# Kernel tuning notes

Hardware: AMD Instinct MI355X
Metric: run time of the kernel (lower is better)

Reference implementation:

```python
import math
import jax, jax.numpy as jnp
import numpy as np

ALPHA, BETA, GAMMA = 1.9, 3.8, 15.2
HEIGHT, WIDTH, SKIP = 32, 32, 1
NUM_HEADS, DIM = 12, 768
HEAD_DIM = DIM // NUM_HEADS


def _piecewise_index_np(rp, alpha, beta, gamma):
    # Eq. (18): identity inside |rp|<=alpha, logarithmic bucketing outside, clipped at beta.
    rp = rp.astype(np.float64)
    rp_abs = np.abs(rp)
    inside = np.round(rp)
    log_part = alpha + np.log(np.maximum(rp_abs, 1e-9) / alpha) / math.log(gamma / alpha) * (beta - alpha)
    outside = np.sign(rp) * np.minimum(np.round(log_part), beta)
    return np.where(rp_abs <= alpha, inside, outside).astype(np.int64)


def _bucket_ids_cross(height, width, skip, alpha, beta, gamma, axis):
    # axis=0 -> CROSS_ROWS, axis=1 -> CROSS_COLS
    rows = np.arange(height)[:, None].repeat(width, 1)
    cols = np.arange(width)[None, :].repeat(height, 0)
    pos = np.stack([rows, cols], 2).reshape(-1, 2)  # [L, 2]
    diff = pos[:, None, axis] - pos[None, :, axis]  # [L, L]
    beta_int = int(beta)
    ids = _piecewise_index_np(diff, alpha, beta, gamma) + beta_int  # in [0, 2*beta_int]
    num_buckets = 2 * beta_int + 1
    L = height * width
    if skip > 0:
        extra = num_buckets
        new_ids = np.full((skip + L, skip + L), extra, dtype=np.int64)
        new_ids[skip:, skip:] = ids
        ids = new_ids
        num_buckets += 1
    return ids.astype(np.int32), num_buckets


def setup_inputs() -> dict:
    key = jax.random.key(0)
    ks = jax.random.split(key, 8)
    N = SKIP + HEIGHT * WIDTH  # 1025
    B = 8
    br, nb = _bucket_ids_cross(HEIGHT, WIDTH, SKIP, ALPHA, BETA, GAMMA, axis=0)
    bc, _ = _bucket_ids_cross(HEIGHT, WIDTH, SKIP, ALPHA, BETA, GAMMA, axis=1)
    w = 0.02
    return {
        "x": jax.random.normal(ks[0], (B, N, DIM), jnp.float32),
        "qkv_w": jax.random.normal(ks[1], (3 * DIM, DIM), jnp.float32) * w,
        "qkv_b": jnp.zeros((3 * DIM,), jnp.float32),
        "proj_w": jax.random.normal(ks[2], (DIM, DIM), jnp.float32) * w,
        "proj_b": jnp.zeros((DIM,), jnp.float32),
        "rpe_rows": jax.random.normal(ks[3], (NUM_HEADS, nb, HEAD_DIM), jnp.float32) * w,
        "rpe_cols": jax.random.normal(ks[4], (NUM_HEADS, nb, HEAD_DIM), jnp.float32) * w,
        "bucket_rows": jnp.asarray(br),
        "bucket_cols": jnp.asarray(bc),
    }


def reference(x, qkv_w, qkv_b, proj_w, proj_b, rpe_rows, rpe_cols, bucket_rows, bucket_cols):
    B, N, C = x.shape
    h = rpe_rows.shape[0]
    d = C // h
    scale = d ** -0.5
    qkv = (x @ qkv_w.T + qkv_b).reshape(B, N, 3, h, d).transpose(2, 0, 3, 1, 4)  # [3,B,h,N,d]
    q, k, v = qkv[0] * scale, qkv[1], qkv[2]
    attn = jnp.einsum('bhid,bhjd->bhij', q, k)  # [B,h,N,N]
    # contextual RPE on keys: project q onto per-head bucket tables, gather per (i,j)
    qt_r = jnp.einsum('bhid,hud->bhiu', q, rpe_rows)  # [B,h,N,nb]
    qt_c = jnp.einsum('bhid,hud->bhiu', q, rpe_cols)
    bias = (jnp.take_along_axis(qt_r, bucket_rows[None, None].astype(jnp.int32), axis=3)
            + jnp.take_along_axis(qt_c, bucket_cols[None, None].astype(jnp.int32), axis=3))
    attn = jax.nn.softmax(attn + bias, axis=-1)
    out = jnp.einsum('bhij,bhjd->bhid', attn, v)
    out = out.transpose(0, 2, 1, 3).reshape(B, N, C)
    return out @ proj_w.T + proj_b
```

## Files before the change

### kernel.cpp

```cpp
#include <hip/hip_runtime.h>

typedef unsigned short u16;
typedef unsigned int   u32;
typedef short  s16x8 __attribute__((ext_vector_type(8)));
typedef float  f32x4 __attribute__((ext_vector_type(4)));

#define B_   8
#define N_   1025
#define H_   12
#define D_   64
#define C_   768
#define NB_  8
#define M_   (B_*N_)
#define QKV_ (3*C_)
#define NEGI -30000.0f
#define LOG2E 1.44269504089f
#define SHIFT2 11.5415603271f
#define CS_  1088

__device__ __forceinline__ float bf2f(u16 u) {
    unsigned int i = ((unsigned int)u) << 16;
    float f; __builtin_memcpy(&f, &i, 4); return f;
}
__device__ __forceinline__ u16 f2bf(float f) {
    unsigned int i; __builtin_memcpy(&i, &f, 4);
    i = (i + 0x7FFFu + ((i >> 16) & 1u)) >> 16;
    return (u16)i;
}
__device__ __forceinline__ float exp2fast(float x) {
#if __has_builtin(__builtin_amdgcn_exp2f)
    return __builtin_amdgcn_exp2f(x);
#else
    float r; asm("v_exp_f32 %0, %1" : "=v"(r) : "v"(x)); return r;
#endif
}

__device__ __forceinline__ void gload_lds16(const u16* gptr, u16* lptr) {
    __builtin_amdgcn_global_load_lds(
        (const __attribute__((address_space(1))) void*)gptr,
        (__attribute__((address_space(3))) void*)lptr, 16, 0, 0);
}

__global__ __launch_bounds__(256)
void cvt_f32_bf16(const float* __restrict__ a, u16* __restrict__ oa, long na,
                  const float* __restrict__ b, u16* __restrict__ ob, long nb,
                  const float* __restrict__ c, u16* __restrict__ oc, long nc)
{
    long t = ((long)blockIdx.x * 256 + threadIdx.x) * 8;
    const float* s; u16* d; long off;
    if (t < na)                 { s = a; d = oa; off = t; }
    else if (t < na + nb)       { s = b; d = ob; off = t - na; }
    else if (t < na + nb + nc)  { s = c; d = oc; off = t - na - nb; }
    else return;
    float4 f0 = *reinterpret_cast<const float4*>(s + off);
    float4 f1 = *reinterpret_cast<const float4*>(s + off + 4);
    u16 tmp[8] = { f2bf(f0.x), f2bf(f0.y), f2bf(f0.z), f2bf(f0.w),
                   f2bf(f1.x), f2bf(f1.y), f2bf(f1.z), f2bf(f1.w) };
    *reinterpret_cast<uint4*>(d + off) = *reinterpret_cast<uint4*>(tmp);
}

__global__ void build_cidx(const int* __restrict__ brow, const int* __restrict__ bcol,
                           unsigned char* __restrict__ cidx) {
    long t = (long)blockIdx.x * 256 + threadIdx.x;
    const long total = (long)CS_ * (CS_ / 4);
    if (t >= total) return;
    int i = (int)(t / (CS_ / 4));
    int k = (int)(t % (CS_ / 4));
    u32 w = 0;
    int p0 = k * 4;
    #pragma unroll
    for (int bnb = 0; bnb < 4; ++bnb) {
        int p = p0 + bnb;
        int jt = p >> 6, rem = p & 63;
        int l = rem >> 2, bn = rem & 3;
        int j = jt * 64 + bn * 16 + l;
        u32 c = 63u;
        if (i < N_ && j < N_) {
            u32 br = (u32)(brow[(size_t)i * N_ + j] & 7);
            u32 bc = (u32)(bcol[(size_t)i * N_ + j] & 7);
            c = (br << 3) | bc;
        }
        w |= c << (8 * bnb);
    }
    ((u32*)cidx)[t] = w;
}

template<int OF32>
__global__ __launch_bounds__(256)
void gemm_bt(const u16* __restrict__ Ap, int lda,
             const u16* __restrict__ Btp,
             const float* __restrict__ bias,
             void* __restrict__ Cout, int ldc,
             int M, int Nn, int K, int scale_cols, float scale_val)
{
    __shared__ u16 As[128][32];
    __shared__ u16 Bs[128][32];
    const int tid  = threadIdx.x;
    const int lane = tid & 63;
    const int wave = tid >> 6;
    const int wm = (wave >> 1) * 64;
    const int wn = (wave & 1) * 64;
    const int m0 = blockIdx.y * 128;
    const int n0 = blockIdx.x * 128;

    const int srow = wave * 16 + (lane >> 2);
    const int scol = (lane & 3) * 8;

    f32x4 acc[4][4] = {};

    for (int k0 = 0; k0 < K; k0 += 32) {
        __syncthreads();
        #pragma unroll
        for (int i = 0; i < 2; ++i) {
            int ar = m0 + i * 64 + srow;
            if (ar > M - 1) ar = M - 1;
            gload_lds16(Ap + (size_t)ar * lda + k0 + scol, &As[i * 64 + wave * 16][0]);
            int br = n0 + i * 64 + srow;
            gload_lds16(Btp + (size_t)br * K + k0 + scol,  &Bs[i * 64 + wave * 16][0]);
        }
        __syncthreads();

        s16x8 af[4], bfv[4];
        #pragma unroll
        for (int qq = 0; qq < 4; ++qq) {
            af[qq]  = *reinterpret_cast<const s16x8*>(&As[wm + qq*16 + (lane & 15)][(lane >> 4) * 8]);
            bfv[qq] = *reinterpret_cast<const s16x8*>(&Bs[wn + qq*16 + (lane & 15)][(lane >> 4) * 8]);
        }
        #pragma unroll
        for (int bm = 0; bm < 4; ++bm)
            #pragma unroll
            for (int bn = 0; bn < 4; ++bn)
                acc[bm][bn] = __builtin_amdgcn_mfma_f32_16x16x32_bf16(af[bm], bfv[bn], acc[bm][bn], 0, 0, 0);
    }

    #pragma unroll
    for (int bm = 0; bm < 4; ++bm) {
        #pragma unroll
        for (int bn = 0; bn < 4; ++bn) {
            int col = n0 + wn + bn*16 + (lane & 15);
            float bv = bias[col];
            float sc = (col < scale_cols) ? scale_val : 1.0f;
            #pragma unroll
            for (int r = 0; r < 4; ++r) {
                int row = m0 + wm + bm*16 + (lane >> 4)*4 + r;
                if (row < M) {
                    float v = (acc[bm][bn][r] + bv) * sc;
                    size_t idx = (size_t)row * ldc + col;
                    if (OF32) ((float*)Cout)[idx] = v;
                    else      ((u16*)Cout)[idx]   = f2bf(v);
                }
            }
        }
    }
}

__global__ __launch_bounds__(512, 4)
void flash_kernel(const u16* __restrict__ qkv,
                  const float* __restrict__ rpe_r, const float* __restrict__ rpe_c,
                  const unsigned char* __restrict__ cidx,
                  u16* __restrict__ aout)
{
    __shared__ u16 Ks[64][72];
    __shared__ u16 Vt[64][72];
    __shared__ u16 Ps[8][16][72];
    __shared__ u16 qtComb[128][72];

    const int tid  = threadIdx.x;
    const int lane = tid & 63;
    const int wave = tid >> 6;
    const int q    = lane >> 4;
    const int l    = lane & 15;
    const int bh = blockIdx.y;
    const int b = bh / H_;
    const int h = bh % H_;
    const int i0 = blockIdx.x * 128;

    float* qtrA = (float*)&Ps[0][0][0];
    float* qtcA = qtrA + 128 * 8;

    {
        int row = tid >> 2;
        int u0  = (tid & 3) * 2;
        int ig = i0 + row;
        bool valid = ig < N_;
        const u16* qrow = &qkv[(size_t)(b * N_ + (valid ? ig : 0)) * QKV_ + h * D_];
        #pragma unroll
        for (int uu = 0; uu < 2; ++uu) {
            int u = u0 + uu;
            const float4* rr4 = (const float4*)&rpe_r[(size_t)(h * NB_ + u) * D_];
            const float4* rc4 = (const float4*)&rpe_c[(size_t)(h * NB_ + u) * D_];
            float sr = 0.f, sc = 0.f;
            #pragma unroll
            for (int e2 = 0; e2 < 8; ++e2) {
                uint4 t = *reinterpret_cast<const uint4*>(&qrow[e2 * 8]);
                s16x8 q8 = *reinterpret_cast<s16x8*>(&t);
                float4 a0 = rr4[2*e2], a1 = rr4[2*e2+1];
                float4 c0 = rc4[2*e2], c1 = rc4[2*e2+1];
                float f0 = bf2f((u16)q8[0]), f1 = bf2f((u16)q8[1]);
                float f2 = bf2f((u16)q8[2]), f3 = bf2f((u16)q8[3]);
                float f4 = bf2f((u16)q8[4]), f5 = bf2f((u16)q8[5]);
                float f6 = bf2f((u16)q8[6]), f7 = bf2f((u16)q8[7]);
                sr += f0*a0.x + f1*a0.y + f2*a0.z + f3*a0.w
                    + f4*a1.x + f5*a1.y + f6*a1.z + f7*a1.w;
                sc += f0*c0.x + f1*c0.y + f2*c0.z + f3*c0.w
                    + f4*c1.x + f5*c1.y + f6*c1.z + f7*c1.w;
            }
            qtrA[row*8 + u] = valid ? sr : 0.f;
            qtcA[row*8 + u] = valid ? sc : 0.f;
        }
    }
    __syncthreads();
    {
        int row = tid >> 2;
        int c0  = (tid & 3) * 16;
        u16 tmp[16];
        #pragma unroll
        for (int cc = 0; cc < 16; ++cc) {
            int c = c0 + cc;
            tmp[cc] = f2bf(qtrA[row*8 + (c >> 3)] + qtcA[row*8 + (c & 7)]);
        }
        *reinterpret_cast<uint4*>(&qtComb[row][c0])     = *reinterpret_cast<uint4*>(&tmp[0]);
        *reinterpret_cast<uint4*>(&qtComb[row][c0 + 8]) = *reinterpret_cast<uint4*>(&tmp[8]);
    }

    s16x8 qf[2];
    {
        int iq = i0 + wave * 16 + l;
        #pragma unroll
        for (int ks = 0; ks < 2; ++ks) {
            uint4 v = make_uint4(0u, 0u, 0u, 0u);
            if (iq < N_)
                v = *reinterpret_cast<const uint4*>(
                    &qkv[(size_t)(b * N_ + iq) * QKV_ + h * D_ + ks * 32 + q * 8]);
            qf[ks] = *reinterpret_cast<s16x8*>(&v);
        }
    }

    float l_part[4] = {0.f, 0.f, 0.f, 0.f};
    f32x4 o_acc[4] = {};

    const int srow = tid >> 3;
    const int g8   = tid & 7;
    const int scol = g8 * 8;
    const int rowq  = wave * 16 + q * 4;
    const int rowq4 = q * 4;

    uint4 kpre, vpre;
    {
        int jg = srow;
        kpre = make_uint4(0u,0u,0u,0u); vpre = make_uint4(0u,0u,0u,0u);
        if (jg < N_) {
            size_t base = (size_t)(b * N_ + jg) * QKV_ + h * D_ + scol;
            kpre = *reinterpret_cast<const uint4*>(&qkv[base + C_]);
            vpre = *reinterpret_cast<const uint4*>(&qkv[base + 2 * C_]);
        }
    }

#define SMAX_BN(bn, MASKED_)                                                  \
    {                                                                         \
        const int jbw = (((bn) << 1) | (l >> 3)) ^ q;                         \
        const int sw = (jbw << 3) | (l & 7);                                  \
        _Pragma("unroll")                                                     \
        for (int r = 0; r < 4; ++r) {                                         \
            int c = (cpk[r] >> ((bn) * 8)) & 63;                              \
            float biasv = bf2f(qtComb[rowq + r][c]);                          \
            float lg = s[bn][r] + biasv;                                      \
            if (MASKED_) { if ((j0 + (bn) * 16 + l) >= N_) lg = NEGI; }       \
            float p = exp2fast(lg);                                           \
            l_part[r] += p;                                                   \
            Ps[wave][rowq4 + r][sw] = f2bf(p);                                \
        }                                                                     \
    }

#define PVHALF(ks)                                                            \
    {                                                                         \
        const int qi = (l >> 2) & 3;                                          \
        s16x8 pf = *reinterpret_cast<const s16x8*>(                           \
            &Ps[wave][l][((((ks) << 2) | q) ^ qi) << 3]);                     \
        _Pragma("unroll")                                                     \
        for (int bn = 0; bn < 4; ++bn) {                                      \
            int gd = ((bn << 1) | (l >> 3)) & 7;                              \
            int jb = (((ks) << 2) | q) ^ gd;                                  \
            s16x8 vf = *reinterpret_cast<const s16x8*>(&Vt[bn * 16 + l][jb << 3]); \
            o_acc[bn] = __builtin_amdgcn_mfma_f32_16x16x32_bf16(pf, vf, o_acc[bn], 0, 0, 0); \
        }                                                                     \
    }

    const int nJT = (N_ + 63) / 64;
    for (int jt = 0; jt < nJT; ++jt) {
        const int j0 = jt * 64;

        u32 cpk[4];
        #pragma unroll
        for (int r = 0; r < 4; ++r) {
            int ig = i0 + wave * 16 + q * 4 + r;
            if (ig > CS_ - 1) ig = CS_ - 1;
            cpk[r] = *reinterpret_cast<const u32*>(&cidx[(size_t)ig * CS_ + j0 + 4 * l]);
        }

        __syncthreads();

        {
            *reinterpret_cast<uint4*>(&Ks[srow][scol]) = kpre;
            s16x8 v8 = *reinterpret_cast<s16x8*>(&vpre);
            int base = (((srow >> 3) ^ g8) << 3) | (srow & 7);
            #pragma unroll
            for (int e = 0; e < 8; ++e) Vt[scol + e][base] = (u16)v8[e];
        }
        {
            int jg = (jt + 1) * 64 + srow;
            kpre = make_uint4(0u,0u,0u,0u); vpre = make_uint4(0u,0u,0u,0u);
            if (jg < N_) {
                size_t base = (size_t)(b * N_ + jg) * QKV_ + h * D_ + scol;
                kpre = *reinterpret_cast<const uint4*>(&qkv[base + C_]);
                vpre = *reinterpret_cast<const uint4*>(&qkv[base + 2 * C_]);
            }
        }
        __syncthreads();

        f32x4 s[4];
        #pragma unroll
        for (int bn = 0; bn < 4; ++bn)
            s[bn] = (f32x4){-SHIFT2, -SHIFT2, -SHIFT2, -SHIFT2};
        #pragma unroll
        for (int bn = 0; bn < 4; ++bn) {
            #pragma unroll
            for (int ks = 0; ks < 2; ++ks) {
                s16x8 kf = *reinterpret_cast<const s16x8*>(&Ks[bn * 16 + l][ks * 32 + q * 8]);
                s[bn] = __builtin_amdgcn_mfma_f32_16x16x32_bf16(qf[ks], kf, s[bn], 0, 0, 0);
            }
        }

        if (jt < nJT - 1) {
            SMAX_BN(0, 0) SMAX_BN(1, 0)
            PVHALF(0)
            SMAX_BN(2, 0) SMAX_BN(3, 0)
            PVHALF(1)
        } else {
            SMAX_BN(0, 1) SMAX_BN(1, 1)
            PVHALF(0)
            SMAX_BN(2, 1) SMAX_BN(3, 1)
            PVHALF(1)
        }
    }

    #pragma unroll
    for (int r = 0; r < 4; ++r) {
        #pragma unroll
        for (int s2 = 1; s2 < 16; s2 <<= 1)
            l_part[r] += __shfl_xor(l_part[r], s2, 64);
    }
    #pragma unroll
    for (int bn = 0; bn < 4; ++bn) {
        #pragma unroll
        for (int r = 0; r < 4; ++r) {
            int ig = i0 + wave * 16 + q * 4 + r;
            if (ig < N_) {
                float lsum = l_part[r];
                float invl = (lsum > 0.f) ? (1.0f / lsum) : 0.f;
                aout[(size_t)(b * N_ + ig) * C_ + h * D_ + bn * 16 + l] = f2bf(o_acc[bn][r] * invl);
            }
        }
    }
#undef SMAX_BN
#undef PVHALF
}

extern "C" void kernel_launch(void* const* d_in, const int* in_sizes, int n_in,
                              void* d_out, int out_size, void* d_ws, size_t ws_size,
                              hipStream_t stream)
{
    const float* x      = (const float*)d_in[0];
    const float* qkv_w  = (const float*)d_in[1];
    const float* qkv_b  = (const float*)d_in[2];
    const float* proj_w = (const float*)d_in[3];
    const float* proj_b = (const float*)d_in[4];
    const float* rpe_r  = (const float*)d_in[5];
    const float* rpe_c  = (const float*)d_in[6];
    const int*   brow   = (const int*)d_in[7];
    const int*   bcol   = (const int*)d_in[8];

    char* p = (char*)d_ws;
    u16* qkv  = (u16*)p; p += (size_t)M_ * QKV_ * 2;
    u16* xaout = (u16*)p; p += (size_t)M_ * C_ * 2;
    unsigned char* cidx = (unsigned char*)p; p += (size_t)CS_ * CS_;
    u16* w1bf = (u16*)p; p += (size_t)QKV_ * C_ * 2;
    u16* w2bf = (u16*)p;

    const long nx = (long)M_ * C_;
    const long n1 = (long)QKV_ * C_;
    const long n2 = (long)C_ * C_;

    cvt_f32_bf16<<<(int)((nx + n1 + n2) / 8 / 256), 256, 0, stream>>>(
        x, xaout, nx, qkv_w, w1bf, n1, proj_w, w2bf, n2);

    build_cidx<<<((CS_ * (CS_ / 4)) + 255) / 256, 256, 0, stream>>>(brow, bcol, cidx);

    gemm_bt<0><<<dim3(QKV_ / 128, (M_ + 127) / 128), 256, 0, stream>>>(
        xaout, C_, w1bf, qkv_b, qkv, QKV_, M_, QKV_, C_, C_, 0.125f * LOG2E);

    flash_kernel<<<dim3((N_ + 127) / 128, B_ * H_), 512, 0, stream>>>(
        qkv, rpe_r, rpe_c, cidx, xaout);

    gemm_bt<1><<<dim3(C_ / 128, (M_ + 127) / 128), 256, 0, stream>>>(
        xaout, C_, w2bf, proj_b, d_out, C_, M_, C_, C_, 0, 1.0f);
}
```

Measured before the change: 316.0 us.

## Process 128-key tiles per barrier pair and raise wave priority around MFMAs

The flash attention loop now stages 128 keys per iteration into enlarged K/V shared buffers, with two 64-key sub-steps in between. This halves the number of `__syncthreads` pairs and global prefetch rounds. Out-of-range prefetch rows are clamped, and the unused second half of the last tile is skipped. `s_setprio` is also raised around the QK and PV MFMA sequences to favour matrix issue across waves. The cost is more shared memory and more prefetch registers, which may reduce occupancy.

```diff
diff --git a/kernel.cpp b/kernel.cpp
--- a/kernel.cpp
+++ b/kernel.cpp
@@ -160,8 +160,8 @@
                   const unsigned char* __restrict__ cidx,
                   u16* __restrict__ aout)
 {
-    __shared__ u16 Ks[64][72];
-    __shared__ u16 Vt[64][72];
+    __shared__ u16 Ks[128][72];
+    __shared__ u16 Vt[64][136];
     __shared__ u16 Ps[8][16][72];
     __shared__ u16 qtComb[128][72];
 
@@ -239,24 +239,22 @@
     float l_part[4] = {0.f, 0.f, 0.f, 0.f};
     f32x4 o_acc[4] = {};
 
-    const int srow = tid >> 3;
+    const int strw = tid >> 3;
     const int g8   = tid & 7;
     const int scol = g8 * 8;
     const int rowq  = wave * 16 + q * 4;
     const int rowq4 = q * 4;
 
-    uint4 kpre, vpre;
-    {
-        int jg = srow;
-        kpre = make_uint4(0u,0u,0u,0u); vpre = make_uint4(0u,0u,0u,0u);
-        if (jg < N_) {
-            size_t base = (size_t)(b * N_ + jg) * QKV_ + h * D_ + scol;
-            kpre = *reinterpret_cast<const uint4*>(&qkv[base + C_]);
-            vpre = *reinterpret_cast<const uint4*>(&qkv[base + 2 * C_]);
-        }
-    }
-
-#define SMAX_BN(bn, MASKED_)                                                  \
+    uint4 kpre[2], vpre[2];
+    #pragma unroll
+    for (int i = 0; i < 2; ++i) {
+        int jg = i * 64 + strw;
+        size_t base = (size_t)(b * N_ + jg) * QKV_ + h * D_ + scol;
+        kpre[i] = *reinterpret_cast<const uint4*>(&qkv[base + C_]);
+        vpre[i] = *reinterpret_cast<const uint4*>(&qkv[base + 2 * C_]);
+    }
+
+#define SMAX_BN(hh, bn, MASKED_)                                              \
     {                                                                         \
         const int jbw = (((bn) << 1) | (l >> 3)) ^ q;                         \
         const int sw = (jbw << 3) | (l & 7);                                  \
@@ -265,30 +263,50 @@
             int c = (cpk[r] >> ((bn) * 8)) & 63;                              \
             float biasv = bf2f(qtComb[rowq + r][c]);                          \
             float lg = s[bn][r] + biasv;                                      \
-            if (MASKED_) { if ((j0 + (bn) * 16 + l) >= N_) lg = NEGI; }       \
+            if (MASKED_) { if ((j0 + (hh)*64 + (bn) * 16 + l) >= N_) lg = NEGI; } \
             float p = exp2fast(lg);                                           \
             l_part[r] += p;                                                   \
             Ps[wave][rowq4 + r][sw] = f2bf(p);                                \
         }                                                                     \
     }
 
-#define PVHALF(ks)                                                            \
+#define PVHALF(hh, ks)                                                        \
     {                                                                         \
         const int qi = (l >> 2) & 3;                                          \
         s16x8 pf = *reinterpret_cast<const s16x8*>(                           \
             &Ps[wave][l][((((ks) << 2) | q) ^ qi) << 3]);                     \
+        __builtin_amdgcn_s_setprio(1);                                        \
         _Pragma("unroll")                                                     \
         for (int bn = 0; bn < 4; ++bn) {                                      \
             int gd = ((bn << 1) | (l >> 3)) & 7;                              \
-            int jb = (((ks) << 2) | q) ^ gd;                                  \
+            int jb = ((hh) << 3) | ((((ks) << 2) | q) ^ gd);                  \
             s16x8 vf = *reinterpret_cast<const s16x8*>(&Vt[bn * 16 + l][jb << 3]); \
             o_acc[bn] = __builtin_amdgcn_mfma_f32_16x16x32_bf16(pf, vf, o_acc[bn], 0, 0, 0); \
         }                                                                     \
-    }
-
-    const int nJT = (N_ + 63) / 64;
+        __builtin_amdgcn_s_setprio(0);                                        \
+    }
+
+#define QKHALF(hh)                                                            \
+    {                                                                         \
+        _Pragma("unroll")                                                     \
+        for (int bn = 0; bn < 4; ++bn)                                        \
+            s[bn] = (f32x4){-SHIFT2, -SHIFT2, -SHIFT2, -SHIFT2};              \
+        __builtin_amdgcn_s_setprio(1);                                        \
+        _Pragma("unroll")                                                     \
+        for (int bn = 0; bn < 4; ++bn) {                                      \
+            _Pragma("unroll")                                                 \
+            for (int ks = 0; ks < 2; ++ks) {                                  \
+                s16x8 kf = *reinterpret_cast<const s16x8*>(                   \
+                    &Ks[(hh) * 64 + bn * 16 + l][ks * 32 + q * 8]);           \
+                s[bn] = __builtin_amdgcn_mfma_f32_16x16x32_bf16(qf[ks], kf, s[bn], 0, 0, 0); \
+            }                                                                 \
+        }                                                                     \
+        __builtin_amdgcn_s_setprio(0);                                        \
+    }
+
+    const int nJT = (N_ + 127) / 128;
     for (int jt = 0; jt < nJT; ++jt) {
-        const int j0 = jt * 64;
+        const int j0 = jt * 128;
 
         u32 cpk[4];
         #pragma unroll
@@ -300,47 +318,52 @@
 
         __syncthreads();
 
-        {
-            *reinterpret_cast<uint4*>(&Ks[srow][scol]) = kpre;
-            s16x8 v8 = *reinterpret_cast<s16x8*>(&vpre);
-            int base = (((srow >> 3) ^ g8) << 3) | (srow & 7);
+        #pragma unroll
+        for (int i = 0; i < 2; ++i) {
+            int row = i * 64 + strw;
+            *reinterpret_cast<uint4*>(&Ks[row][scol]) = kpre[i];
+            s16x8 v8 = *reinterpret_cast<s16x8*>(&vpre[i]);
+            int base = (((row >> 3) ^ g8) << 3) | (row & 7);
             #pragma unroll
             for (int e = 0; e < 8; ++e) Vt[scol + e][base] = (u16)v8[e];
         }
-        {
-            int jg = (jt + 1) * 64 + srow;
-            kpre = make_uint4(0u,0u,0u,0u); vpre = make_uint4(0u,0u,0u,0u);
-            if (jg < N_) {
+        if (jt + 1 < nJT) {
+            #pragma unroll
+            for (int i = 0; i < 2; ++i) {
+                int jg = (jt + 1) * 128 + i * 64 + strw;
+                if (jg > N_ - 1) jg = N_ - 1;
                 size_t base = (size_t)(b * N_ + jg) * QKV_ + h * D_ + scol;
-                kpre = *reinterpret_cast<const uint4*>(&qkv[base + C_]);
-                vpre = *reinterpret_cast<const uint4*>(&qkv[base + 2 * C_]);
+                kpre[i] = *reinterpret_cast<const uint4*>(&qkv[base + C_]);
+                vpre[i] = *reinterpret_cast<const uint4*>(&qkv[base + 2 * C_]);
             }
         }
         __syncthreads();
 
         f32x4 s[4];
-        #pragma unroll
-        for (int bn = 0; bn < 4; ++bn)
-            s[bn] = (f32x4){-SHIFT2, -SHIFT2, -SHIFT2, -SHIFT2};
-        #pragma unroll
-        for (int bn = 0; bn < 4; ++bn) {
-            #pragma unroll
-            for (int ks = 0; ks < 2; ++ks) {
-                s16x8 kf = *reinterpret_cast<const s16x8*>(&Ks[bn * 16 + l][ks * 32 + q * 8]);
-                s[bn] = __builtin_amdgcn_mfma_f32_16x16x32_bf16(qf[ks], kf, s[bn], 0, 0, 0);
+        QKHALF(0)
+        if (jt < nJT - 1) {
+            SMAX_BN(0, 0, 0) SMAX_BN(0, 1, 0)
+            PVHALF(0, 0)
+            SMAX_BN(0, 2, 0) SMAX_BN(0, 3, 0)
+            PVHALF(0, 1)
+        } else {
+            SMAX_BN(0, 0, 1) SMAX_BN(0, 1, 1)
+            PVHALF(0, 0)
+            SMAX_BN(0, 2, 1) SMAX_BN(0, 3, 1)
+            PVHALF(0, 1)
+        }
+        if (jt < nJT - 1) {
+            #pragma unroll
+            for (int r = 0; r < 4; ++r) {
+                int ig = i0 + wave * 16 + q * 4 + r;
+                if (ig > CS_ - 1) ig = CS_ - 1;
+                cpk[r] = *reinterpret_cast<const u32*>(&cidx[(size_t)ig * CS_ + j0 + 64 + 4 * l]);
             }
-        }
-
-        if (jt < nJT - 1) {
-            SMAX_BN(0, 0) SMAX_BN(1, 0)
-            PVHALF(0)
-            SMAX_BN(2, 0) SMAX_BN(3, 0)
-            PVHALF(1)
-        } else {
-            SMAX_BN(0, 1) SMAX_BN(1, 1)
-            PVHALF(0)
-            SMAX_BN(2, 1) SMAX_BN(3, 1)
-            PVHALF(1)
+            QKHALF(1)
+            SMAX_BN(1, 0, 0) SMAX_BN(1, 1, 0)
+            PVHALF(1, 0)
+            SMAX_BN(1, 2, 0) SMAX_BN(1, 3, 0)
+            PVHALF(1, 1)
         }
     }
 
@@ -364,6 +387,7 @@
     }
 #undef SMAX_BN
 #undef PVHALF
+#undef QKHALF
 }
 
 extern "C" void kernel_launch(void* const* d_in, const int* in_sizes, int n_in,
```

Result: slower. 345.5 us (+9.4%).
